# Kernel optimization log

Measured on AMD Instinct MI355X. Metric: run time of the kernel, lower is better.

## Reference

```python
import jax, jax.numpy as jnp
import numpy as np

N = 100000   # nodes
E = 1600000  # edges
G = 512      # graphs in batch
IN_C, H1, H2, OUT_C = 3, 64, 128, 2


def setup_inputs() -> dict:
    key = jax.random.key(0)
    ks = jax.random.split(key, 9)
    x = jax.random.normal(ks[0], (N, IN_C), dtype=jnp.float32)
    edge_index = jax.random.randint(ks[1], (2, E), 0, N, dtype=jnp.int64)
    batch = jnp.sort(jax.random.randint(ks[2], (N,), 0, G, dtype=jnp.int64))
    # Glorot-ish init for weights, zeros for biases (as PyG GCNConv / nn.Linear defaults roughly)
    def glorot(k, shape):
        lim = float(np.sqrt(6.0 / (shape[0] + shape[1])))
        return jax.random.uniform(k, shape, jnp.float32, -lim, lim)
    W1 = glorot(ks[3], (IN_C, H1)); b1 = jnp.zeros((H1,), jnp.float32)
    W2 = glorot(ks[4], (H1, H2));   b2 = jnp.zeros((H2,), jnp.float32)
    Wfc = glorot(ks[5], (H2, OUT_C)); bfc = jnp.zeros((OUT_C,), jnp.float32)
    return {"x": x, "edge_index": edge_index, "batch": batch,
            "W1": W1, "b1": b1, "W2": W2, "b2": b2, "Wfc": Wfc, "bfc": bfc}


def _gcn_conv(x, W, b, src, dst, dinv):
    # PyG GCNConv: out = D^{-1/2} (A + I) D^{-1/2} X W + b
    xw = x @ W                                    # [N, F]
    norm = dinv[src] * dinv[dst]                  # per-edge symmetric norm
    agg = jax.ops.segment_sum(norm[:, None] * xw[src], dst, num_segments=x.shape[0])
    agg = agg + (dinv * dinv)[:, None] * xw       # self-loop contribution
    return agg + b


def reference(x, edge_index, batch, W1, b1, W2, b2, Wfc, bfc):
    src, dst = edge_index[0], edge_index[1]
    # degree with self-loops (edge weight 1), counted at edge targets as in PyG
    deg = jax.ops.segment_sum(jnp.ones((E,), x.dtype), dst, num_segments=N) + 1.0
    dinv = jax.lax.rsqrt(deg)
    h = jax.nn.relu(_gcn_conv(x, W1, b1, src, dst, dinv))
    h = jax.nn.relu(_gcn_conv(h, W2, b2, src, dst, dinv))
    # global_mean_pool over batch indices
    sums = jax.ops.segment_sum(h, batch, num_segments=G)          # [G, H2]
    cnt = jax.ops.segment_sum(jnp.ones((N,), h.dtype), batch, num_segments=G)
    pooled = sums / jnp.maximum(cnt, 1.0)[:, None]
    return pooled @ Wfc + bfc
```

## Files before the change

### kernel.cpp

```cpp
#include <hip/hip_runtime.h>

#define NN 100000
#define NE 1600000
#define NG 512
#define C_H1 64
#define C_H2 128
#define C_OUT 2

#define MM2_BLOCKS ((NN + 127) / 128)
#define NB ((NN + 255) >> 8)
#define PCHUNKS 512
#define PCHUNK_E (NE / PCHUNKS)
#define AT2_S 36

__global__ void k_hist(const int* __restrict__ ei, int* __restrict__ hist) {
    __shared__ int lh[NB];
    int tid = threadIdx.x;
    int blk = blockIdx.x;
    for (int i = tid; i < NB; i += 256) lh[i] = 0;
    __syncthreads();
    int base = blk * PCHUNK_E;
    for (int e = base + tid; e < base + PCHUNK_E; e += 256)
        atomicAdd(&lh[ei[NE + e] >> 8], 1);
    __syncthreads();
    for (int i = tid; i < NB; i += 256) hist[i * PCHUNKS + blk] = lh[i];
}

__global__ void k_colscan0(const int* __restrict__ hist, int* __restrict__ offs,
                           int* __restrict__ btot) {
    __shared__ int sh[256];
    int b = blockIdx.x;
    int tid = threadIdx.x;
    int v0 = hist[b * PCHUNKS + 2 * tid];
    int v1 = hist[b * PCHUNKS + 2 * tid + 1];
    sh[tid] = v0 + v1;
    __syncthreads();
    for (int off = 1; off < 256; off <<= 1) {
        int v = (tid >= off) ? sh[tid - off] : 0;
        __syncthreads();
        sh[tid] += v;
        __syncthreads();
    }
    int base = (tid == 0) ? 0 : sh[tid - 1];
    offs[b * PCHUNKS + 2 * tid]     = base;
    offs[b * PCHUNKS + 2 * tid + 1] = base + v0;
    if (tid == 255) btot[b] = sh[255];
}

__global__ void k_bbase(const int* __restrict__ btot, int* __restrict__ bbase,
                        int* __restrict__ row_ptr) {
    __shared__ int sh[256];
    int tid = threadIdx.x;
    int v0 = (2 * tid     < NB) ? btot[2 * tid]     : 0;
    int v1 = (2 * tid + 1 < NB) ? btot[2 * tid + 1] : 0;
    sh[tid] = v0 + v1;
    __syncthreads();
    for (int off = 1; off < 256; off <<= 1) {
        int v = (tid >= off) ? sh[tid - off] : 0;
        __syncthreads();
        sh[tid] += v;
        __syncthreads();
    }
    int base = (tid == 0) ? 0 : sh[tid - 1];
    if (2 * tid     < NB) bbase[2 * tid]     = base;
    if (2 * tid + 1 < NB) bbase[2 * tid + 1] = base + v0;
    if (tid == 255) { bbase[NB] = sh[255]; row_ptr[NN] = sh[255]; }
}

__global__ void k_scatterA(const int* __restrict__ ei, const int* __restrict__ offs,
                           const int* __restrict__ bbase, int2* __restrict__ ed2) {
    __shared__ int lcur[NB];
    int tid = threadIdx.x;
    int blk = blockIdx.x;
    for (int i = tid; i < NB; i += 256) lcur[i] = bbase[i] + offs[i * PCHUNKS + blk];
    __syncthreads();
    int base = blk * PCHUNK_E;
    for (int e = base + tid; e < base + PCHUNK_E; e += 256) {
        int s = ei[e], d = ei[NE + e];
        int pos = atomicAdd(&lcur[d >> 8], 1);
        int2 v; v.x = s; v.y = d;
        ed2[pos] = v;
    }
}

__global__ void k_B1(const int2* __restrict__ ed2, const int* __restrict__ bbase,
                     float* __restrict__ dinv, int* __restrict__ row_ptr) {
    __shared__ int ldeg[256];
    __shared__ int sh[256];
    int b = blockIdx.x;
    int tid = threadIdx.x;
    int lo = b << 8;
    ldeg[tid] = 0;
    __syncthreads();
    int beg = bbase[b], end = bbase[b + 1];
    for (int j = beg + tid; j < end; j += 256)
        atomicAdd(&ldeg[ed2[j].y - lo], 1);
    __syncthreads();
    int d = ldeg[tid];
    int node = lo + tid;
    if (node < NN) dinv[node] = rsqrtf((float)d + 1.0f);
    sh[tid] = d;
    __syncthreads();
    for (int off = 1; off < 256; off <<= 1) {
        int v = (tid >= off) ? sh[tid - off] : 0;
        __syncthreads();
        sh[tid] += v;
        __syncthreads();
    }
    int excl = beg + ((tid == 0) ? 0 : sh[tid - 1]);
    if (node < NN) row_ptr[node] = excl;
}

__global__ void k_x4(const float* __restrict__ x, float4* __restrict__ x4) {
    int n = blockIdx.x * blockDim.x + threadIdx.x;
    if (n >= NN) return;
    float4 v; v.x = x[n * 3]; v.y = x[n * 3 + 1]; v.z = x[n * 3 + 2]; v.w = 0.f;
    x4[n] = v;
}

__global__ void k_scatterB(const int* __restrict__ row_ptr, const int2* __restrict__ ed2,
                           const float* __restrict__ dinv, const float4* __restrict__ x4,
                           int* __restrict__ ed, float4* __restrict__ aggx4) {
    __shared__ int   lcur[256];
    __shared__ float ldin[256];
    __shared__ float lax[256 * 3];
    int b = blockIdx.x;
    int lo = b << 8;
    int tid = threadIdx.x;
    int node = lo + tid;
    if (node <= NN) lcur[tid] = row_ptr[node < NN ? node : NN];
    else            lcur[tid] = 0;
    ldin[tid] = (node < NN) ? dinv[node] : 0.f;
    lax[tid] = 0.f; lax[256 + tid] = 0.f; lax[512 + tid] = 0.f;
    __syncthreads();
    int seg_beg = row_ptr[lo];
    int hi = lo + 256; if (hi > NN) hi = NN;
    int seg_end = row_ptr[hi];
    for (int j = seg_beg + tid; j < seg_end; j += 256) {
        int2 sd = ed2[j];
        int local = sd.y - lo;
        int pos = atomicAdd(&lcur[local], 1);
        float nrm = dinv[sd.x] * ldin[local];
        ed[pos] = sd.x;
        float4 xs = x4[sd.x];
        atomicAdd(&lax[local],       nrm * xs.x);
        atomicAdd(&lax[256 + local], nrm * xs.y);
        atomicAdd(&lax[512 + local], nrm * xs.z);
    }
    __syncthreads();
    if (node < NN) {
        float di = ldin[tid];
        float s2 = di * di;
        float4 xs = x4[node];
        float4 a;
        a.x = lax[tid]       + s2 * xs.x;
        a.y = lax[256 + tid] + s2 * xs.y;
        a.z = lax[512 + tid] + s2 * xs.z;
        a.w = di;
        aggx4[node] = a;
    }
}

__global__ void k_edge1(const int* __restrict__ row_ptr, const int* __restrict__ ed,
                        const float4* __restrict__ aggx4,
                        const float* __restrict__ W1, const float* __restrict__ b1,
                        float* __restrict__ agg1) {
    __shared__ float4 lp[256];
    int t = blockIdx.x * 256 + threadIdx.x;
    int n = t >> 6, c = t & 63;
    int lane = threadIdx.x & 63;
    int wbase = threadIdx.x & 192;

    float w0 = W1[c], w1 = W1[64 + c], w2 = W1[128 + c], bb = b1[c];
    float4 an = aggx4[n];
    float di = an.w;
    float hself = fmaxf(fmaf(an.x, w0, fmaf(an.y, w1, fmaf(an.z, w2, bb))), 0.f);
    float acc = di * di * hself;

    int beg = row_ptr[n], end = row_ptr[n + 1];
    for (int base = beg; base < end; base += 64) {
        int m = end - base; if (m > 64) m = 64;
        if (lane < m) {
            int s = ed[base + lane];
            float4 ax = aggx4[s];
            float4 p; p.x = ax.x; p.y = ax.y; p.z = ax.z; p.w = ax.w * di;
            lp[wbase + lane] = p;
        }
        int e = 0;
        for (; e + 3 < m; e += 4) {
            float4 p0 = lp[wbase + e];
            float4 p1 = lp[wbase + e + 1];
            float4 p2 = lp[wbase + e + 2];
            float4 p3 = lp[wbase + e + 3];
            float h0  = fmaxf(fmaf(p0.x, w0, fmaf(p0.y, w1, fmaf(p0.z, w2, bb))), 0.f);
            float h1v = fmaxf(fmaf(p1.x, w0, fmaf(p1.y, w1, fmaf(p1.z, w2, bb))), 0.f);
            float h2v = fmaxf(fmaf(p2.x, w0, fmaf(p2.y, w1, fmaf(p2.z, w2, bb))), 0.f);
            float h3v = fmaxf(fmaf(p3.x, w0, fmaf(p3.y, w1, fmaf(p3.z, w2, bb))), 0.f);
            acc = fmaf(p0.w, h0, acc);
            acc = fmaf(p1.w, h1v, acc);
            acc = fmaf(p2.w, h2v, acc);
            acc = fmaf(p3.w, h3v, acc);
        }
        for (; e < m; ++e) {
            float4 p = lp[wbase + e];
            float h = fmaxf(fmaf(p.x, w0, fmaf(p.y, w1, fmaf(p.z, w2, bb))), 0.f);
            acc = fmaf(p.w, h, acc);
        }
    }
    agg1[t] = acc;
}

__global__ __launch_bounds__(256)
void k_mm2pool(const float* __restrict__ agg1, const float* __restrict__ W2,
               const float* __restrict__ b2, const int* __restrict__ batch,
               float* __restrict__ pooled) {
    __shared__ float wt[C_H1 * C_H2];
    __shared__ float at[128 * AT2_S];
    __shared__ float lpool[4 * C_H2];
    int tid = threadIdx.x;
    int bx  = blockIdx.x;

    {
        const float4* w4 = (const float4*)W2;
        float4* wl = (float4*)wt;
        for (int i = tid; i < (C_H1 * C_H2) / 4; i += 256) wl[i] = w4[i];
        for (int i = tid; i < 4 * C_H2; i += 256) lpool[i] = 0.f;
    }

    int tx = tid & 15;
    int my = tid >> 4;
    int c0 = tx * 4;

    float acc[8][8];
#pragma unroll
    for (int i = 0; i < 8; ++i)
#pragma unroll
        for (int j = 0; j < 8; ++j) acc[i][j] = 0.f;

    const float4* a4 = (const float4*)(agg1 + (size_t)bx * 128 * C_H1);

#pragma unroll 1
    for (int h = 0; h < 2; ++h) {
        __syncthreads();
        for (int i = tid; i < 128 * 8; i += 256) {
            int row = i >> 3, q = i & 7;
            *(float4*)&at[row * AT2_S + q * 4] = a4[row * 16 + h * 8 + q];
        }
        __syncthreads();
        int kb = h * 32;
        for (int k0 = 0; k0 < 32; k0 += 4) {
            float4 wfA[4], wfB[4];
#pragma unroll
            for (int kk = 0; kk < 4; ++kk) {
                wfA[kk] = *(const float4*)&wt[(kb + k0 + kk) * C_H2 + c0];
                wfB[kk] = *(const float4*)&wt[(kb + k0 + kk) * C_H2 + 64 + c0];
            }
#pragma unroll
            for (int i = 0; i < 8; ++i) {
                float4 af = *(const float4*)&at[(my + i * 16) * AT2_S + k0];
#pragma unroll
                for (int kk = 0; kk < 4; ++kk) {
                    float a = (kk == 0) ? af.x : (kk == 1) ? af.y : (kk == 2) ? af.z : af.w;
                    acc[i][0] = fmaf(a, wfA[kk].x, acc[i][0]);
                    acc[i][1] = fmaf(a, wfA[kk].y, acc[i][1]);
                    acc[i][2] = fmaf(a, wfA[kk].z, acc[i][2]);
                    acc[i][3] = fmaf(a, wfA[kk].w, acc[i][3]);
                    acc[i][4] = fmaf(a, wfB[kk].x, acc[i][4]);
                    acc[i][5] = fmaf(a, wfB[kk].y, acc[i][5]);
                    acc[i][6] = fmaf(a, wfB[kk].z, acc[i][6]);
                    acc[i][7] = fmaf(a, wfB[kk].w, acc[i][7]);
                }
            }
        }
    }

    int nbase = bx * 128;
    int gbase = batch[nbase];
    int gidx[8];
#pragma unroll
    for (int i = 0; i < 8; ++i) {
        int node = nbase + my + i * 16;
        gidx[i] = (node < NN) ? batch[node] : -1;
    }

#pragma unroll
    for (int j = 0; j < 8; ++j) {
        int c = (j < 4) ? (c0 + j) : (64 + c0 + j - 4);
        float bb = b2[c];
        int run_g = -1;
        float rs = 0.f;
#pragma unroll
        for (int i = 0; i < 8; ++i) {
            if (gidx[i] < 0) break;
            float hcur = fmaxf(acc[i][j] + bb, 0.f);
            if (gidx[i] != run_g) {
                if (run_g >= 0) {
                    int slot = run_g - gbase;
                    if (slot < 4) atomicAdd(&lpool[slot * C_H2 + c], rs);
                    else          atomicAdd(&pooled[(run_g << 7) + c], rs);
                }
                run_g = gidx[i]; rs = hcur;
            } else {
                rs += hcur;
            }
        }
        if (run_g >= 0) {
            int slot = run_g - gbase;
            if (slot < 4) atomicAdd(&lpool[slot * C_H2 + c], rs);
            else          atomicAdd(&pooled[(run_g << 7) + c], rs);
        }
    }
    __syncthreads();
    for (int i = tid; i < 4 * C_H2; i += 256) {
        int slot = i >> 7, c = i & 127;
        int g = gbase + slot;
        float v = lpool[i];
        if (g < NG && v != 0.f) atomicAdd(&pooled[(g << 7) + c], v);
    }
}

__device__ __forceinline__ int lower_bound(const int* __restrict__ a, int n, int key) {
    int lo = 0, hi = n;
    while (lo < hi) { int mid = (lo + hi) >> 1; if (a[mid] < key) lo = mid + 1; else hi = mid; }
    return lo;
}

__global__ void k_fc(const float* __restrict__ pooled, const int* __restrict__ batch,
                     const float* __restrict__ Wfc, const float* __restrict__ bfc,
                     float* __restrict__ out) {
    int t = blockIdx.x * blockDim.x + threadIdx.x;
    if (t >= NG * C_OUT) return;
    int g = t >> 1, o = t & 1;
    int start = lower_bound(batch, NN, g);
    int end   = lower_bound(batch, NN, g + 1);
    float inv = 1.f / fmaxf((float)(end - start), 1.f);
    float s = bfc[o];
    for (int cc = 0; cc < C_H2; ++cc)
        s = fmaf(pooled[(g << 7) + cc] * inv, Wfc[cc * C_OUT + o], s);
    out[t] = s;
}

extern "C" void kernel_launch(void* const* d_in, const int* in_sizes, int n_in,
                              void* d_out, int out_size, void* d_ws, size_t ws_size,
                              hipStream_t stream) {
    const float* x     = (const float*)d_in[0];
    const int*   ei    = (const int*)d_in[1];
    const int*   batch = (const int*)d_in[2];
    const float* W1    = (const float*)d_in[3];
    const float* b1    = (const float*)d_in[4];
    const float* W2    = (const float*)d_in[5];
    const float* b2    = (const float*)d_in[6];
    const float* Wfc   = (const float*)d_in[7];
    const float* bfc   = (const float*)d_in[8];
    float* out = (float*)d_out;

    char* p = (char*)d_ws;
    auto alloc = [&](size_t bytes) { char* r = p; p += (bytes + 255) & ~size_t(255); return r; };
    float*  dinv    = (float*) alloc((size_t)NN * 4);
    int*    row_ptr = (int*)   alloc((size_t)(NN + 1) * 4);
    int*    btot    = (int*)   alloc((size_t)NB * 4);
    int*    bbase   = (int*)   alloc((size_t)(NB + 1) * 4);
    int*    hist    = (int*)   alloc((size_t)NB * PCHUNKS * 4);
    int*    offs    = (int*)   alloc((size_t)NB * PCHUNKS * 4);
    int2*   ed2     = (int2*)  alloc((size_t)NE * 8);
    int*    ed      = (int*)   alloc((size_t)NE * 4);
    float4* x4      = (float4*)alloc((size_t)NN * 16);
    float4* aggx4   = (float4*)alloc((size_t)NN * 16);
    float*  agg1    = (float*) alloc((size_t)(NN + 128) * C_H1 * 4);
    float*  pooled  = (float*) alloc((size_t)NG * C_H2 * 4);

    hipMemsetAsync(pooled, 0, (size_t)NG * C_H2 * 4, stream);
    k_hist    <<<PCHUNKS, 256, 0, stream>>>(ei, hist);
    k_colscan0<<<NB, 256, 0, stream>>>(hist, offs, btot);
    k_bbase   <<<1, 256, 0, stream>>>(btot, bbase, row_ptr);
    k_scatterA<<<PCHUNKS, 256, 0, stream>>>(ei, offs, bbase, ed2);
    k_B1      <<<NB, 256, 0, stream>>>(ed2, bbase, dinv, row_ptr);
    k_x4      <<<(NN + 255) / 256, 256, 0, stream>>>(x, x4);
    k_scatterB<<<NB, 256, 0, stream>>>(row_ptr, ed2, dinv, x4, ed, aggx4);
    k_edge1   <<<(NN * C_H1) / 256, 256, 0, stream>>>(row_ptr, ed, aggx4, W1, b1, agg1);
    k_mm2pool <<<MM2_BLOCKS, 256, 0, stream>>>(agg1, W2, b2, batch, pooled);
    k_fc      <<<(NG * C_OUT + 255) / 256, 256, 0, stream>>>(pooled, batch, Wfc, bfc, out);
}
```

Baseline: 234.6 us.

## Shrink node buckets to 64 and read agg1 directly from global in mm2pool

Node buckets for the CSR build drop from 256 to 64 nodes, so there are four times as many scatterB and B1 blocks, more parallelism and less LDS atomic contention per bucket. The bucket-base scan now handles up to 2048 buckets by giving each thread eight entries. Separately, the matmul-pool kernel stops staging agg1 tiles in shared memory and loads float4 rows straight from global, cutting LDS use and two barriers per half. The trade-off is redundant global/L2 reads of agg1 across the 16 column threads, and many small blocks that use only 64 of 256 threads in some phases.

```diff
diff --git a/kernel.cpp b/kernel.cpp
--- a/kernel.cpp
+++ b/kernel.cpp
@@ -8,10 +8,11 @@
 #define C_OUT 2
 
 #define MM2_BLOCKS ((NN + 127) / 128)
-#define NB ((NN + 255) >> 8)
+#define BSH 6
+#define BSZ 64
+#define NB ((NN + BSZ - 1) >> BSH)
 #define PCHUNKS 512
 #define PCHUNK_E (NE / PCHUNKS)
-#define AT2_S 36
 
 __global__ void k_hist(const int* __restrict__ ei, int* __restrict__ hist) {
     __shared__ int lh[NB];
@@ -21,7 +22,7 @@
     __syncthreads();
     int base = blk * PCHUNK_E;
     for (int e = base + tid; e < base + PCHUNK_E; e += 256)
-        atomicAdd(&lh[ei[NE + e] >> 8], 1);
+        atomicAdd(&lh[ei[NE + e] >> BSH], 1);
     __syncthreads();
     for (int i = tid; i < NB; i += 256) hist[i * PCHUNKS + blk] = lh[i];
 }
@@ -51,19 +52,29 @@
                         int* __restrict__ row_ptr) {
     __shared__ int sh[256];
     int tid = threadIdx.x;
-    int v0 = (2 * tid     < NB) ? btot[2 * tid]     : 0;
-    int v1 = (2 * tid + 1 < NB) ? btot[2 * tid + 1] : 0;
-    sh[tid] = v0 + v1;
+    int v[8];
+    int s = 0;
+#pragma unroll
+    for (int j = 0; j < 8; ++j) {
+        int idx = tid * 8 + j;
+        v[j] = (idx < NB) ? btot[idx] : 0;
+        s += v[j];
+    }
+    sh[tid] = s;
     __syncthreads();
     for (int off = 1; off < 256; off <<= 1) {
-        int v = (tid >= off) ? sh[tid - off] : 0;
-        __syncthreads();
-        sh[tid] += v;
+        int t = (tid >= off) ? sh[tid - off] : 0;
+        __syncthreads();
+        sh[tid] += t;
         __syncthreads();
     }
     int base = (tid == 0) ? 0 : sh[tid - 1];
-    if (2 * tid     < NB) bbase[2 * tid]     = base;
-    if (2 * tid + 1 < NB) bbase[2 * tid + 1] = base + v0;
+#pragma unroll
+    for (int j = 0; j < 8; ++j) {
+        int idx = tid * 8 + j;
+        if (idx < NB) bbase[idx] = base;
+        base += v[j];
+    }
     if (tid == 255) { bbase[NB] = sh[255]; row_ptr[NN] = sh[255]; }
 }
 
@@ -77,7 +88,7 @@
     int base = blk * PCHUNK_E;
     for (int e = base + tid; e < base + PCHUNK_E; e += 256) {
         int s = ei[e], d = ei[NE + e];
-        int pos = atomicAdd(&lcur[d >> 8], 1);
+        int pos = atomicAdd(&lcur[d >> BSH], 1);
         int2 v; v.x = s; v.y = d;
         ed2[pos] = v;
     }
@@ -85,30 +96,30 @@
 
 __global__ void k_B1(const int2* __restrict__ ed2, const int* __restrict__ bbase,
                      float* __restrict__ dinv, int* __restrict__ row_ptr) {
-    __shared__ int ldeg[256];
-    __shared__ int sh[256];
+    __shared__ int ldeg[BSZ];
+    __shared__ int sh[BSZ];
     int b = blockIdx.x;
     int tid = threadIdx.x;
-    int lo = b << 8;
-    ldeg[tid] = 0;
+    int lo = b << BSH;
+    if (tid < BSZ) ldeg[tid] = 0;
     __syncthreads();
     int beg = bbase[b], end = bbase[b + 1];
     for (int j = beg + tid; j < end; j += 256)
         atomicAdd(&ldeg[ed2[j].y - lo], 1);
     __syncthreads();
-    int d = ldeg[tid];
+    int d = (tid < BSZ) ? ldeg[tid] : 0;
     int node = lo + tid;
-    if (node < NN) dinv[node] = rsqrtf((float)d + 1.0f);
-    sh[tid] = d;
-    __syncthreads();
-    for (int off = 1; off < 256; off <<= 1) {
-        int v = (tid >= off) ? sh[tid - off] : 0;
-        __syncthreads();
-        sh[tid] += v;
-        __syncthreads();
-    }
-    int excl = beg + ((tid == 0) ? 0 : sh[tid - 1]);
-    if (node < NN) row_ptr[node] = excl;
+    if (tid < BSZ && node < NN) dinv[node] = rsqrtf((float)d + 1.0f);
+    if (tid < BSZ) sh[tid] = d;
+    __syncthreads();
+    for (int off = 1; off < BSZ; off <<= 1) {
+        int v = (tid >= off && tid < BSZ) ? sh[tid - off] : 0;
+        __syncthreads();
+        if (tid < BSZ) sh[tid] += v;
+        __syncthreads();
+    }
+    if (tid < BSZ && node < NN)
+        row_ptr[node] = beg + ((tid == 0) ? 0 : sh[tid - 1]);
 }
 
 __global__ void k_x4(const float* __restrict__ x, float4* __restrict__ x4) {
@@ -121,20 +132,21 @@
 __global__ void k_scatterB(const int* __restrict__ row_ptr, const int2* __restrict__ ed2,
                            const float* __restrict__ dinv, const float4* __restrict__ x4,
                            int* __restrict__ ed, float4* __restrict__ aggx4) {
-    __shared__ int   lcur[256];
-    __shared__ float ldin[256];
-    __shared__ float lax[256 * 3];
+    __shared__ int   lcur[BSZ];
+    __shared__ float ldin[BSZ];
+    __shared__ float lax[BSZ * 3];
     int b = blockIdx.x;
-    int lo = b << 8;
-    int tid = threadIdx.x;
-    int node = lo + tid;
-    if (node <= NN) lcur[tid] = row_ptr[node < NN ? node : NN];
-    else            lcur[tid] = 0;
-    ldin[tid] = (node < NN) ? dinv[node] : 0.f;
-    lax[tid] = 0.f; lax[256 + tid] = 0.f; lax[512 + tid] = 0.f;
-    __syncthreads();
+    int lo = b << BSH;
+    int tid = threadIdx.x;
+    if (tid < BSZ) {
+        int node = lo + tid;
+        lcur[tid] = row_ptr[node < NN ? node : NN];
+        ldin[tid] = (node < NN) ? dinv[node] : 0.f;
+        lax[tid] = 0.f; lax[BSZ + tid] = 0.f; lax[2 * BSZ + tid] = 0.f;
+    }
+    __syncthreads();
+    int hi = lo + BSZ; if (hi > NN) hi = NN;
     int seg_beg = row_ptr[lo];
-    int hi = lo + 256; if (hi > NN) hi = NN;
     int seg_end = row_ptr[hi];
     for (int j = seg_beg + tid; j < seg_end; j += 256) {
         int2 sd = ed2[j];
@@ -143,21 +155,24 @@
         float nrm = dinv[sd.x] * ldin[local];
         ed[pos] = sd.x;
         float4 xs = x4[sd.x];
-        atomicAdd(&lax[local],       nrm * xs.x);
-        atomicAdd(&lax[256 + local], nrm * xs.y);
-        atomicAdd(&lax[512 + local], nrm * xs.z);
-    }
-    __syncthreads();
-    if (node < NN) {
-        float di = ldin[tid];
-        float s2 = di * di;
-        float4 xs = x4[node];
-        float4 a;
-        a.x = lax[tid]       + s2 * xs.x;
-        a.y = lax[256 + tid] + s2 * xs.y;
-        a.z = lax[512 + tid] + s2 * xs.z;
-        a.w = di;
-        aggx4[node] = a;
+        atomicAdd(&lax[local],           nrm * xs.x);
+        atomicAdd(&lax[BSZ + local],     nrm * xs.y);
+        atomicAdd(&lax[2 * BSZ + local], nrm * xs.z);
+    }
+    __syncthreads();
+    if (tid < BSZ) {
+        int node = lo + tid;
+        if (node < NN) {
+            float di = ldin[tid];
+            float s2 = di * di;
+            float4 xs = x4[node];
+            float4 a;
+            a.x = lax[tid]           + s2 * xs.x;
+            a.y = lax[BSZ + tid]     + s2 * xs.y;
+            a.z = lax[2 * BSZ + tid] + s2 * xs.z;
+            a.w = di;
+            aggx4[node] = a;
+        }
     }
 }
 
@@ -215,7 +230,6 @@
                const float* __restrict__ b2, const int* __restrict__ batch,
                float* __restrict__ pooled) {
     __shared__ float wt[C_H1 * C_H2];
-    __shared__ float at[128 * AT2_S];
     __shared__ float lpool[4 * C_H2];
     int tid = threadIdx.x;
     int bx  = blockIdx.x;
@@ -226,6 +240,7 @@
         for (int i = tid; i < (C_H1 * C_H2) / 4; i += 256) wl[i] = w4[i];
         for (int i = tid; i < 4 * C_H2; i += 256) lpool[i] = 0.f;
     }
+    __syncthreads();
 
     int tx = tid & 15;
     int my = tid >> 4;
@@ -237,39 +252,30 @@
 #pragma unroll
         for (int j = 0; j < 8; ++j) acc[i][j] = 0.f;
 
-    const float4* a4 = (const float4*)(agg1 + (size_t)bx * 128 * C_H1);
+    const float* ab = agg1 + (size_t)bx * 128 * C_H1;
 
 #pragma unroll 1
-    for (int h = 0; h < 2; ++h) {
-        __syncthreads();
-        for (int i = tid; i < 128 * 8; i += 256) {
-            int row = i >> 3, q = i & 7;
-            *(float4*)&at[row * AT2_S + q * 4] = a4[row * 16 + h * 8 + q];
-        }
-        __syncthreads();
-        int kb = h * 32;
-        for (int k0 = 0; k0 < 32; k0 += 4) {
-            float4 wfA[4], wfB[4];
+    for (int k0 = 0; k0 < C_H1; k0 += 4) {
+        float4 wfA[4], wfB[4];
+#pragma unroll
+        for (int kk = 0; kk < 4; ++kk) {
+            wfA[kk] = *(const float4*)&wt[(k0 + kk) * C_H2 + c0];
+            wfB[kk] = *(const float4*)&wt[(k0 + kk) * C_H2 + 64 + c0];
+        }
+#pragma unroll
+        for (int i = 0; i < 8; ++i) {
+            float4 af = *(const float4*)(ab + (my + i * 16) * C_H1 + k0);
 #pragma unroll
             for (int kk = 0; kk < 4; ++kk) {
-                wfA[kk] = *(const float4*)&wt[(kb + k0 + kk) * C_H2 + c0];
-                wfB[kk] = *(const float4*)&wt[(kb + k0 + kk) * C_H2 + 64 + c0];
-            }
-#pragma unroll
-            for (int i = 0; i < 8; ++i) {
-                float4 af = *(const float4*)&at[(my + i * 16) * AT2_S + k0];
-#pragma unroll
-                for (int kk = 0; kk < 4; ++kk) {
-                    float a = (kk == 0) ? af.x : (kk == 1) ? af.y : (kk == 2) ? af.z : af.w;
-                    acc[i][0] = fmaf(a, wfA[kk].x, acc[i][0]);
-                    acc[i][1] = fmaf(a, wfA[kk].y, acc[i][1]);
-                    acc[i][2] = fmaf(a, wfA[kk].z, acc[i][2]);
-                    acc[i][3] = fmaf(a, wfA[kk].w, acc[i][3]);
-                    acc[i][4] = fmaf(a, wfB[kk].x, acc[i][4]);
-                    acc[i][5] = fmaf(a, wfB[kk].y, acc[i][5]);
-                    acc[i][6] = fmaf(a, wfB[kk].z, acc[i][6]);
-                    acc[i][7] = fmaf(a, wfB[kk].w, acc[i][7]);
-                }
+                float a = (kk == 0) ? af.x : (kk == 1) ? af.y : (kk == 2) ? af.z : af.w;
+                acc[i][0] = fmaf(a, wfA[kk].x, acc[i][0]);
+                acc[i][1] = fmaf(a, wfA[kk].y, acc[i][1]);
+                acc[i][2] = fmaf(a, wfA[kk].z, acc[i][2]);
+                acc[i][3] = fmaf(a, wfA[kk].w, acc[i][3]);
+                acc[i][4] = fmaf(a, wfB[kk].x, acc[i][4]);
+                acc[i][5] = fmaf(a, wfB[kk].y, acc[i][5]);
+                acc[i][6] = fmaf(a, wfB[kk].z, acc[i][6]);
+                acc[i][7] = fmaf(a, wfB[kk].w, acc[i][7]);
             }
         }
     }
```

Result: slower. 246.3 us (+5.0%).

## Stream agg1 rows directly into registers with prefetch in layer-2 matmul

Applied to the files above, without the earlier changes.

Removes the shared-memory staging tile for agg1 in the fused matmul+pool kernel. Each thread now loads its own rows from global memory as float4s, double-buffered in registers so the next k-slice is fetched while the current one is multiplied. This drops two barriers per half and frees LDS, which may raise occupancy. In exchange it issues strided, less coalesced global loads (each thread reads 16 bytes at a 256-byte row stride) and uses more registers for the prefetch buffers.

```diff
diff --git a/kernel.cpp b/kernel.cpp
--- a/kernel.cpp
+++ b/kernel.cpp
@@ -11,7 +11,6 @@
 #define NB ((NN + 255) >> 8)
 #define PCHUNKS 512
 #define PCHUNK_E (NE / PCHUNKS)
-#define AT2_S 36
 
 __global__ void k_hist(const int* __restrict__ ei, int* __restrict__ hist) {
     __shared__ int lh[NB];
@@ -215,7 +214,6 @@
                const float* __restrict__ b2, const int* __restrict__ batch,
                float* __restrict__ pooled) {
     __shared__ float wt[C_H1 * C_H2];
-    __shared__ float at[128 * AT2_S];
     __shared__ float lpool[4 * C_H2];
     int tid = threadIdx.x;
     int bx  = blockIdx.x;
@@ -226,6 +224,7 @@
         for (int i = tid; i < (C_H1 * C_H2) / 4; i += 256) wl[i] = w4[i];
         for (int i = tid; i < 4 * C_H2; i += 256) lpool[i] = 0.f;
     }
+    __syncthreads();
 
     int tx = tid & 15;
     int my = tid >> 4;
@@ -237,41 +236,41 @@
 #pragma unroll
         for (int j = 0; j < 8; ++j) acc[i][j] = 0.f;
 
-    const float4* a4 = (const float4*)(agg1 + (size_t)bx * 128 * C_H1);
+    const float* ab = agg1 + (size_t)bx * 128 * C_H1;
+
+    float4 cur[8], nxt[8];
+#pragma unroll
+    for (int i = 0; i < 8; ++i)
+        cur[i] = *(const float4*)(ab + (my + i * 16) * C_H1);
 
 #pragma unroll 1
-    for (int h = 0; h < 2; ++h) {
-        __syncthreads();
-        for (int i = tid; i < 128 * 8; i += 256) {
-            int row = i >> 3, q = i & 7;
-            *(float4*)&at[row * AT2_S + q * 4] = a4[row * 16 + h * 8 + q];
-        }
-        __syncthreads();
-        int kb = h * 32;
-        for (int k0 = 0; k0 < 32; k0 += 4) {
-            float4 wfA[4], wfB[4];
-#pragma unroll
-            for (int kk = 0; kk < 4; ++kk) {
-                wfA[kk] = *(const float4*)&wt[(kb + k0 + kk) * C_H2 + c0];
-                wfB[kk] = *(const float4*)&wt[(kb + k0 + kk) * C_H2 + 64 + c0];
+    for (int k0 = 0; k0 < C_H1; k0 += 4) {
+        int kn = k0 + 4;
+        if (kn < C_H1) {
+#pragma unroll
+            for (int i = 0; i < 8; ++i)
+                nxt[i] = *(const float4*)(ab + (my + i * 16) * C_H1 + kn);
+        }
+#pragma unroll
+        for (int kk = 0; kk < 4; ++kk) {
+            float4 wA = *(const float4*)&wt[(k0 + kk) * C_H2 + c0];
+            float4 wB = *(const float4*)&wt[(k0 + kk) * C_H2 + 64 + c0];
+#pragma unroll
+            for (int i = 0; i < 8; ++i) {
+                float a = (kk == 0) ? cur[i].x : (kk == 1) ? cur[i].y
+                        : (kk == 2) ? cur[i].z : cur[i].w;
+                acc[i][0] = fmaf(a, wA.x, acc[i][0]);
+                acc[i][1] = fmaf(a, wA.y, acc[i][1]);
+                acc[i][2] = fmaf(a, wA.z, acc[i][2]);
+                acc[i][3] = fmaf(a, wA.w, acc[i][3]);
+                acc[i][4] = fmaf(a, wB.x, acc[i][4]);
+                acc[i][5] = fmaf(a, wB.y, acc[i][5]);
+                acc[i][6] = fmaf(a, wB.z, acc[i][6]);
+                acc[i][7] = fmaf(a, wB.w, acc[i][7]);
             }
-#pragma unroll
-            for (int i = 0; i < 8; ++i) {
-                float4 af = *(const float4*)&at[(my + i * 16) * AT2_S + k0];
-#pragma unroll
-                for (int kk = 0; kk < 4; ++kk) {
-                    float a = (kk == 0) ? af.x : (kk == 1) ? af.y : (kk == 2) ? af.z : af.w;
-                    acc[i][0] = fmaf(a, wfA[kk].x, acc[i][0]);
-                    acc[i][1] = fmaf(a, wfA[kk].y, acc[i][1]);
-                    acc[i][2] = fmaf(a, wfA[kk].z, acc[i][2]);
-                    acc[i][3] = fmaf(a, wfA[kk].w, acc[i][3]);
-                    acc[i][4] = fmaf(a, wfB[kk].x, acc[i][4]);
-                    acc[i][5] = fmaf(a, wfB[kk].y, acc[i][5]);
-                    acc[i][6] = fmaf(a, wfB[kk].z, acc[i][6]);
-                    acc[i][7] = fmaf(a, wfB[kk].w, acc[i][7]);
-                }
-            }
-        }
+        }
+#pragma unroll
+        for (int i = 0; i < 8; ++i) cur[i] = nxt[i];
     }
 
     int nbase = bx * 128;
```

After: 235.9 us. About the same (+0.5%).

## Swizzle edge1/mm2pool blocks per XCD and read agg1 directly from global

Applied to the files above, without the earlier changes.

Remaps k_edge1 block indices so that every 128-node tile is produced by blocks on the same XCD that will later run the matching k_mm2pool block. The aim is to keep the agg1 intermediate resident in that XCD's L2 between the two kernels. k_mm2pool also drops its LDS staging of agg1 and loads float4s straight from global memory, which removes two barriers and the shared-memory copy. The trade-off is that the GEMM inner loop now does repeated strided global loads that depend on cache hits, and both grids are padded with early-exit blocks.

```diff
diff --git a/kernel.cpp b/kernel.cpp
--- a/kernel.cpp
+++ b/kernel.cpp
@@ -8,10 +8,10 @@
 #define C_OUT 2
 
 #define MM2_BLOCKS ((NN + 127) / 128)
+#define MM2_PAD 784
 #define NB ((NN + 255) >> 8)
 #define PCHUNKS 512
 #define PCHUNK_E (NE / PCHUNKS)
-#define AT2_S 36
 
 __global__ void k_hist(const int* __restrict__ ei, int* __restrict__ hist) {
     __shared__ int lh[NB];
@@ -166,8 +166,14 @@
                         const float* __restrict__ W1, const float* __restrict__ b1,
                         float* __restrict__ agg1) {
     __shared__ float4 lp[256];
-    int t = blockIdx.x * 256 + threadIdx.x;
-    int n = t >> 6, c = t & 63;
+    int bsw = blockIdx.x;
+    int r   = bsw & 7;
+    int idx = bsw >> 3;
+    int T   = r + ((idx >> 5) << 3);
+    int nb  = (T << 5) + (idx & 31);
+    int n   = (nb << 2) + (threadIdx.x >> 6);
+    if (n >= NN) return;
+    int c = threadIdx.x & 63;
     int lane = threadIdx.x & 63;
     int wbase = threadIdx.x & 192;
 
@@ -207,18 +213,21 @@
             acc = fmaf(p.w, h, acc);
         }
     }
-    agg1[t] = acc;
+    agg1[n * 64 + c] = acc;
 }
 
 __global__ __launch_bounds__(256)
 void k_mm2pool(const float* __restrict__ agg1, const float* __restrict__ W2,
                const float* __restrict__ b2, const int* __restrict__ batch,
                float* __restrict__ pooled) {
+    int bsw = blockIdx.x;
+    int bx  = (bsw & 7) + ((bsw >> 3) << 3 == 0 ? 0 : ((bsw >> 3) << 3));
+    bx = (bsw & 7) + ((bsw >> 3) << 3);
+    if (bx >= MM2_BLOCKS) return;
+
     __shared__ float wt[C_H1 * C_H2];
-    __shared__ float at[128 * AT2_S];
     __shared__ float lpool[4 * C_H2];
     int tid = threadIdx.x;
-    int bx  = blockIdx.x;
 
     {
         const float4* w4 = (const float4*)W2;
@@ -226,6 +235,7 @@
         for (int i = tid; i < (C_H1 * C_H2) / 4; i += 256) wl[i] = w4[i];
         for (int i = tid; i < 4 * C_H2; i += 256) lpool[i] = 0.f;
     }
+    __syncthreads();
 
     int tx = tid & 15;
     int my = tid >> 4;
@@ -237,39 +247,30 @@
 #pragma unroll
         for (int j = 0; j < 8; ++j) acc[i][j] = 0.f;
 
-    const float4* a4 = (const float4*)(agg1 + (size_t)bx * 128 * C_H1);
+    const float* ab = agg1 + (size_t)bx * 128 * C_H1;
 
 #pragma unroll 1
-    for (int h = 0; h < 2; ++h) {
-        __syncthreads();
-        for (int i = tid; i < 128 * 8; i += 256) {
-            int row = i >> 3, q = i & 7;
-            *(float4*)&at[row * AT2_S + q * 4] = a4[row * 16 + h * 8 + q];
-        }
-        __syncthreads();
-        int kb = h * 32;
-        for (int k0 = 0; k0 < 32; k0 += 4) {
-            float4 wfA[4], wfB[4];
+    for (int k0 = 0; k0 < C_H1; k0 += 4) {
+        float4 wfA[4], wfB[4];
+#pragma unroll
+        for (int kk = 0; kk < 4; ++kk) {
+            wfA[kk] = *(const float4*)&wt[(k0 + kk) * C_H2 + c0];
+            wfB[kk] = *(const float4*)&wt[(k0 + kk) * C_H2 + 64 + c0];
+        }
+#pragma unroll
+        for (int i = 0; i < 8; ++i) {
+            float4 af = *(const float4*)(ab + (my + i * 16) * C_H1 + k0);
 #pragma unroll
             for (int kk = 0; kk < 4; ++kk) {
-                wfA[kk] = *(const float4*)&wt[(kb + k0 + kk) * C_H2 + c0];
-                wfB[kk] = *(const float4*)&wt[(kb + k0 + kk) * C_H2 + 64 + c0];
-            }
-#pragma unroll
-            for (int i = 0; i < 8; ++i) {
-                float4 af = *(const float4*)&at[(my + i * 16) * AT2_S + k0];
-#pragma unroll
-                for (int kk = 0; kk < 4; ++kk) {
-                    float a = (kk == 0) ? af.x : (kk == 1) ? af.y : (kk == 2) ? af.z : af.w;
-                    acc[i][0] = fmaf(a, wfA[kk].x, acc[i][0]);
-                    acc[i][1] = fmaf(a, wfA[kk].y, acc[i][1]);
-                    acc[i][2] = fmaf(a, wfA[kk].z, acc[i][2]);
-                    acc[i][3] = fmaf(a, wfA[kk].w, acc[i][3]);
-                    acc[i][4] = fmaf(a, wfB[kk].x, acc[i][4]);
-                    acc[i][5] = fmaf(a, wfB[kk].y, acc[i][5]);
-                    acc[i][6] = fmaf(a, wfB[kk].z, acc[i][6]);
-                    acc[i][7] = fmaf(a, wfB[kk].w, acc[i][7]);
-                }
+                float a = (kk == 0) ? af.x : (kk == 1) ? af.y : (kk == 2) ? af.z : af.w;
+                acc[i][0] = fmaf(a, wfA[kk].x, acc[i][0]);
+                acc[i][1] = fmaf(a, wfA[kk].y, acc[i][1]);
+                acc[i][2] = fmaf(a, wfA[kk].z, acc[i][2]);
+                acc[i][3] = fmaf(a, wfA[kk].w, acc[i][3]);
+                acc[i][4] = fmaf(a, wfB[kk].x, acc[i][4]);
+                acc[i][5] = fmaf(a, wfB[kk].y, acc[i][5]);
+                acc[i][6] = fmaf(a, wfB[kk].z, acc[i][6]);
+                acc[i][7] = fmaf(a, wfB[kk].w, acc[i][7]);
             }
         }
     }
@@ -377,7 +378,7 @@
     k_B1      <<<NB, 256, 0, stream>>>(ed2, bbase, dinv, row_ptr);
     k_x4      <<<(NN + 255) / 256, 256, 0, stream>>>(x, x4);
     k_scatterB<<<NB, 256, 0, stream>>>(row_ptr, ed2, dinv, x4, ed, aggx4);
-    k_edge1   <<<(NN * C_H1) / 256, 256, 0, stream>>>(row_ptr, ed, aggx4, W1, b1, agg1);
-    k_mm2pool <<<MM2_BLOCKS, 256, 0, stream>>>(agg1, W2, b2, batch, pooled);
+    k_edge1   <<<MM2_PAD * 32, 256, 0, stream>>>(row_ptr, ed, aggx4, W1, b1, agg1);
+    k_mm2pool <<<MM2_PAD, 256, 0, stream>>>(agg1, W2, b2, batch, pooled);
     k_fc      <<<(NG * C_OUT + 255) / 256, 256, 0, stream>>>(pooled, batch, Wfc, bfc, out);
 }
```

After: 237.5 us. Within noise of the previous version (+1.2%).
